# Kernel tuning notes

Hardware: AMD Instinct MI355X
Metric: run time of the kernel (lower is better)

## Reference

```python
import math
import jax, jax.numpy as jnp
import numpy as np

B, T, C, H, D = 2, 2048, 1024, 16, 64


def make_rope_cache(seq_len, head_dim, base=10000.0):
    half = head_dim // 2
    inv_freq = 1.0 / (base ** (np.arange(0, half, dtype=np.float32) / half))
    t = np.arange(seq_len, dtype=np.float32)
    freqs = np.outer(t, inv_freq)  # (T, D/2)
    cache = np.stack([np.cos(freqs), np.sin(freqs)], axis=1)  # (T, 2, D/2)
    return jnp.asarray(cache, dtype=jnp.float32)


def setup_inputs() -> dict:
    key = jax.random.key(0)
    ks = jax.random.split(key, 6)
    s = 1.0 / math.sqrt(C)
    return {
        "x": jax.random.normal(ks[0], (B, T, C), dtype=jnp.float32),
        "rope_cache": make_rope_cache(T, D),
        "Wq": jax.random.normal(ks[1], (C, C), dtype=jnp.float32) * s,
        "Wk": jax.random.normal(ks[2], (C, C), dtype=jnp.float32) * s,
        "Wv": jax.random.normal(ks[3], (C, C), dtype=jnp.float32) * s,
        "Wo": jax.random.normal(ks[4], (C, C), dtype=jnp.float32) * s,
        "mask": jnp.ones((B, T), dtype=jnp.bool_),
    }


def apply_rope(x, rope_cache):
    # x: (B, T, H, D); rope_cache: (T, 2, D//2)
    seq_len = x.shape[1]
    cos = rope_cache[:seq_len, 0, :][None, :, None, :]
    sin = rope_cache[:seq_len, 1, :][None, :, None, :]
    half = x.shape[-1] // 2
    x1, x2 = x[..., :half], x[..., half:]
    return jnp.concatenate([x1 * cos - x2 * sin, x1 * sin + x2 * cos], axis=-1)


def reference(x, rope_cache, Wq, Wk, Wv, Wo, mask):
    b, t, c = x.shape
    q = (x @ Wq).reshape(b, t, H, D)
    k = (x @ Wk).reshape(b, t, H, D)
    v = (x @ Wv).reshape(b, t, H, D)
    q = apply_rope(q, rope_cache).transpose(0, 2, 1, 3)  # (B,H,T,D)
    k = apply_rope(k, rope_cache).transpose(0, 2, 1, 3)
    v = v.transpose(0, 2, 1, 3)
    scale = 1.0 / math.sqrt(D)
    attn = jnp.einsum('bhid,bhjd->bhij', q, k) * scale  # (B,H,T,T)
    causal = jnp.tril(jnp.ones((t, t), dtype=jnp.bool_))
    attn = jnp.where(causal[None, None, :, :], attn, -1e9)
    attn = jnp.where(mask[:, None, None, :], attn, -1e9)
    attn = jax.nn.softmax(attn, axis=-1)
    out = jnp.einsum('bhij,bhjd->bhid', attn, v)
    out = out.transpose(0, 2, 1, 3).reshape(b, t, c)
    return out @ Wo
```

## Files before the change

kernel.cpp:

```cpp
#include <hip/hip_runtime.h>


typedef short s16x8 __attribute__((ext_vector_type(8)));
typedef __bf16 bf16x8 __attribute__((ext_vector_type(8)));
typedef float f32x4 __attribute__((ext_vector_type(4)));
typedef float f32x16 __attribute__((ext_vector_type(16)));
typedef unsigned u32x4 __attribute__((ext_vector_type(4)));
typedef unsigned u32x2 __attribute__((ext_vector_type(2)));

__device__ __forceinline__ short f2bf(float f) {
  unsigned u = __builtin_bit_cast(unsigned, f);
  u += 0x7fffu + ((u >> 16) & 1u);
  return (short)(u >> 16);
}

__device__ __forceinline__ unsigned cvtpk(float lo, float hi) {
  unsigned r;
  asm("v_cvt_pk_bf16_f32 %0, %1, %2" : "=v"(r) : "v"(lo), "v"(hi));
  return r;
}

__device__ __forceinline__ f32x4 mfma16(s16x8 a, s16x8 b, f32x4 c) {
  return __builtin_amdgcn_mfma_f32_16x16x32_bf16(
      __builtin_bit_cast(bf16x8, a), __builtin_bit_cast(bf16x8, b), c, 0, 0, 0);
}

__device__ __forceinline__ f32x16 mfma32(s16x8 a, s16x8 b, f32x16 c) {
  return __builtin_amdgcn_mfma_f32_32x32x16_bf16(
      __builtin_bit_cast(bf16x8, a), __builtin_bit_cast(bf16x8, b), c, 0, 0, 0);
}

__device__ __forceinline__ void gload16(const void* g, void* l) {
  __builtin_amdgcn_global_load_lds(
      (__attribute__((address_space(1))) void*)(void*)g,
      (__attribute__((address_space(3))) void*)l, 16, 0, 0);
}

__global__ void cvt_fused_kernel(const float* __restrict__ xin,
                                 const float* __restrict__ Wq, const float* __restrict__ Wk,
                                 const float* __restrict__ Wv, const float* __restrict__ Wo,
                                 short* __restrict__ xb, short* __restrict__ wt) {
  __shared__ float t32[32][33];
  int bid = blockIdx.x;
  int tid = threadIdx.x;
  if (bid < 2048) {
    int i = bid * 256 + tid;
    const float4* p = (const float4*)xin + (size_t)i * 2;
    float4 a = p[0], b = p[1];
    s16x8 o;
    o[0] = f2bf(a.x); o[1] = f2bf(a.y); o[2] = f2bf(a.z); o[3] = f2bf(a.w);
    o[4] = f2bf(b.x); o[5] = f2bf(b.y); o[6] = f2bf(b.z); o[7] = f2bf(b.w);
    ((s16x8*)xb)[i] = o;
  } else {
    int b = bid - 2048;
    int z = b >> 10;
    int rem = b & 1023;
    int n0 = (rem & 31) * 32, k0 = (rem >> 5) * 32;
    const float* W = (z == 0) ? Wq : (z == 1) ? Wk : (z == 2) ? Wv : Wo;
    short* o = wt + (size_t)z * 1024 * 1024;
    int tx = tid & 31, ty = tid >> 5;
#pragma unroll
    for (int i = 0; i < 4; ++i) t32[ty + 8 * i][tx] = W[(size_t)(k0 + ty + 8 * i) * 1024 + n0 + tx];
    __syncthreads();
#pragma unroll
    for (int i = 0; i < 4; ++i) o[(size_t)(n0 + ty + 8 * i) * 1024 + k0 + tx] = f2bf(t32[tx][ty + 8 * i]);
  }
}

__global__ __launch_bounds__(256) void qkv_gemm_kernel(
    const short* __restrict__ xb, const short* __restrict__ wt,
    const float* __restrict__ rope,
    short* __restrict__ Qo, short* __restrict__ Ko, short* __restrict__ Vt) {
  __shared__ short As[2][128 * 64];
  __shared__ short Bs[2][64 * 64];
  int bid = blockIdx.x;
  int wgid = (bid & 7) * 192 + (bid >> 3);
  int mt = wgid / 48;
  int ntile = wgid % 48;
  int mat = ntile >> 4;
  int h = ntile & 15;
  int tid = threadIdx.x, lane = tid & 63, w = tid >> 6;
  int rloc = lane & 15, lgrp = lane >> 4;
  int e3 = rloc & 7;

  const char* Agb0 = (const char*)(xb + (size_t)mt * 128 * 1024);
  const char* Bgb0 = (const char*)(wt + (size_t)mat * 1024 * 1024 + (size_t)h * 64 * 1024);

  f32x4 acc[2][4];
#pragma unroll
  for (int m = 0; m < 2; ++m)
#pragma unroll
    for (int n = 0; n < 4; ++n) acc[m][n] = (f32x4){0.f, 0.f, 0.f, 0.f};

  auto STAGE = [&](int buf, int kt) {
    const char* Ag = Agb0 + kt * 128;
    const char* Bg = Bgb0 + kt * 128;
    char* ad = (char*)&As[buf][0];
    char* bd = (char*)&Bs[buf][0];
#pragma unroll
    for (int rr = 0; rr < 4; ++rr) {
      int lin = rr * 4096 + tid * 16;
      int row = lin >> 7;
      int ch = (lin >> 4) & 7;
      int srcoff = (row << 11) + ((ch ^ (row & 7)) << 4);
      gload16(Ag + srcoff, ad + lin);
    }
#pragma unroll
    for (int rr = 0; rr < 2; ++rr) {
      int lin = rr * 4096 + tid * 16;
      int row = lin >> 7;
      int ch = (lin >> 4) & 7;
      int srcoff = (row << 11) + ((ch ^ (row & 7)) << 4);
      gload16(Bg + srcoff, bd + lin);
    }
  };

  STAGE(0, 0);
  for (int kt = 0; kt < 16; ++kt) {
    int cur = kt & 1;
    if (kt + 1 < 16) {
      STAGE(cur ^ 1, kt + 1);
      asm volatile("s_waitcnt vmcnt(6)" ::: "memory");
    } else {
      asm volatile("s_waitcnt vmcnt(0)" ::: "memory");
    }
    __builtin_amdgcn_s_barrier();
#pragma unroll
    for (int kk = 0; kk < 2; ++kk) {
      s16x8 a[2], b[4];
#pragma unroll
      for (int m = 0; m < 2; ++m)
        a[m] = *(const s16x8*)&As[cur][(w * 32 + m * 16 + rloc) * 64 + (((kk * 4 + lgrp) ^ e3) << 3)];
#pragma unroll
      for (int n = 0; n < 4; ++n)
        b[n] = *(const s16x8*)&Bs[cur][(n * 16 + rloc) * 64 + (((kk * 4 + lgrp) ^ e3) << 3)];
      __builtin_amdgcn_s_setprio(1);
#pragma unroll
      for (int m = 0; m < 2; ++m)
#pragma unroll
        for (int n = 0; n < 4; ++n) acc[m][n] = mfma16(a[m], b[n], acc[m][n]);
      __builtin_amdgcn_s_setprio(0);
    }
    __builtin_amdgcn_s_barrier();
  }

  if (mat < 2) {
    bool isK = (mat == 1);
    float csf = isK ? 1.0f : (0.125f * 1.44269504088896340736f);
    short* dst = (mat == 0) ? Qo : Ko;
#pragma unroll
    for (int m = 0; m < 2; ++m) {
#pragma unroll
      for (int j = 0; j < 4; ++j) {
        int rowg = mt * 128 + w * 32 + m * 16 + lgrp * 4 + j;
        int bI = rowg >> 11, t = rowg & 2047;
        short* hb = dst + (((size_t)(bI * 16 + h)) * 2048 + t) * 64;
#pragma unroll
        for (int n = 0; n < 2; ++n) {
          int d = n * 16 + rloc;
          float cs = rope[t * 64 + d] * csf;
          float sn = rope[t * 64 + 32 + d] * csf;
          float a0 = acc[m][n][j], b0 = acc[m][n + 2][j];
          int d2 = d + 32;
          int a1 = isK ? ((((d >> 3) ^ (t & 7)) << 3) | (d & 7)) : d;
          int a2 = isK ? ((((d2 >> 3) ^ (t & 7)) << 3) | (d & 7)) : d2;
          hb[a1] = f2bf(a0 * cs - b0 * sn);
          hb[a2] = f2bf(a0 * sn + b0 * cs);
        }
      }
    }
  } else {
    __syncthreads();
    short* T = &As[0][0];
#pragma unroll
    for (int m = 0; m < 2; ++m)
#pragma unroll
      for (int j = 0; j < 4; ++j) {
        int t_in = w * 32 + m * 16 + lgrp * 4 + j;
#pragma unroll
        for (int n = 0; n < 4; ++n) {
          int d = n * 16 + rloc;
          T[t_in * 66 + d] = f2bf(acc[m][n][j]);
        }
      }
    __syncthreads();
    int d = tid & 63;
    int th = tid >> 6;
    int t0g = mt * 128;
    int bI = t0g >> 11;
    short* vrow = Vt + (((size_t)(bI * 16 + h)) * 64 + d) * 2048 + (t0g & 2047);
#pragma unroll
    for (int c = 0; c < 4; ++c) {
      int tw0 = th * 32 + c * 8;
      s16x8 pk;
#pragma unroll
      for (int i = 0; i < 8; ++i) pk[i] = T[(tw0 + i) * 66 + d];
      int gr = (((tw0 >> 3) & 15) ^ (d & 15)) << 3;
      *(s16x8*)(vrow + gr) = pk;
    }
  }
}

__global__ __launch_bounds__(256, 2) void attn_kernel(
    const short* __restrict__ Q, const short* __restrict__ K,
    const short* __restrict__ Vt, short* __restrict__ O) {
  __shared__ short Ks[4][64 * 64];
  __shared__ short Vs[4][64 * 64];
  int tid = threadIdx.x;
  int lane = tid & 63;
  int w = tid >> 6;
  int bh = blockIdx.x;
  int qb = 15 - (int)blockIdx.y;
  int qv = lane & 31, h = lane >> 5;
  int q0 = qb * 128 + w * 32;
  int tq = q0 + qv;

  const short* Qg = Q + ((size_t)bh * 2048 + q0) * 64;
  s16x8 qf[4];
#pragma unroll
  for (int kq = 0; kq < 4; ++kq)
    qf[kq] = *(const s16x8*)(Qg + qv * 64 + kq * 16 + h * 8);

  const char* KgB = (const char*)(K + (size_t)bh * 2048 * 64);
  const char* VgB = (const char*)(Vt + (size_t)bh * 64 * 2048);

  f32x16 l_acc;
  f32x16 ot0, ot1;
#pragma unroll
  for (int r = 0; r < 16; ++r) { ot0[r] = 0.f; ot1[r] = 0.f; l_acc[r] = 0.f; }

  int nkv = 2 * qb + 2;

  auto STAGE = [&](int slot, int kt) {
    int k0 = kt << 6;
    const char* Kg = KgB + (size_t)k0 * 128;
    char* kd = (char*)&Ks[slot][0];
    char* vd = (char*)&Vs[slot][0];
    gload16(Kg + tid * 16, kd + tid * 16);
    gload16(Kg + 4096 + tid * 16, kd + 4096 + tid * 16);
    size_t vwin = (size_t)((k0 & ~127) * 2);
    int kpar = (k0 >> 6) & 1;
    {
      int lin = tid * 16;
      int d = lin >> 7, col = lin & 127;
      int ho = (((d >> 3) & 1) ^ kpar) << 7;
      gload16(VgB + (size_t)d * 4096 + vwin + ho + col, vd + lin);
    }
    {
      int lin = 4096 + tid * 16;
      int d = lin >> 7, col = lin & 127;
      int ho = (((d >> 3) & 1) ^ kpar) << 7;
      gload16(VgB + (size_t)d * 4096 + vwin + ho + col, vd + lin);
    }
  };

  STAGE(0, 0);
  STAGE(1, 1);

  for (int kt = 0; kt < nkv; ++kt) {
    int b = kt & 3;
    int k0 = kt << 6;
    if (kt + 2 < nkv) STAGE((kt + 2) & 3, kt + 2);
    if (kt + 2 < nkv)      asm volatile("s_waitcnt vmcnt(8)" ::: "memory");
    else if (kt + 1 < nkv) asm volatile("s_waitcnt vmcnt(4)" ::: "memory");
    else                   asm volatile("s_waitcnt vmcnt(0)" ::: "memory");
    __builtin_amdgcn_s_barrier();

    bool act = (k0 <= q0 + 31);
    if (act) {
      f32x16 s[2];
#pragma unroll
      for (int n = 0; n < 2; ++n)
#pragma unroll
        for (int r = 0; r < 16; ++r) s[n][r] = 0.f;
      __builtin_amdgcn_s_setprio(1);
#pragma unroll
      for (int n = 0; n < 2; ++n) {
        int r = n * 32 + qv;
#pragma unroll
        for (int kq = 0; kq < 4; ++kq) {
          s16x8 ka = *(const s16x8*)&Ks[b][r * 64 + (((2 * kq + h) ^ (r & 7)) << 3)];
          s[n] = mfma32(ka, qf[kq], s[n]);
        }
      }
      __builtin_amdgcn_s_setprio(0);
      if (k0 + 63 > q0) {
#pragma unroll
        for (int n = 0; n < 2; ++n)
#pragma unroll
          for (int r = 0; r < 16; ++r) {
            int tk = k0 + n * 32 + (r & 3) + ((r >> 2) << 3) + h * 4;
            if (tk > tq) s[n][r] = -3.0e38f;
          }
      }
#pragma unroll
      for (int n = 0; n < 2; ++n)
#pragma unroll
        for (int r = 0; r < 16; ++r)
          s[n][r] = exp2f(s[n][r]);
      l_acc += s[0] + s[1];

#pragma unroll
      for (int n = 0; n < 2; ++n) {
        unsigned dA[4], dB[4];
#pragma unroll
        for (int m = 0; m < 4; ++m) {
          dA[m] = cvtpk(s[n][4 * m], s[n][4 * m + 1]);
          dB[m] = cvtpk(s[n][4 * m + 2], s[n][4 * m + 3]);
        }
#pragma unroll
        for (int c = 0; c < 2; ++c) {
          u32x4 fv;
#if __has_builtin(__builtin_amdgcn_permlane32_swap)
          u32x2 pa = __builtin_amdgcn_permlane32_swap(dA[2 * c], dA[2 * c + 1], false, false);
          u32x2 pb = __builtin_amdgcn_permlane32_swap(dB[2 * c], dB[2 * c + 1], false, false);
          fv[0] = pa[0]; fv[1] = pb[0]; fv[2] = pa[1]; fv[3] = pb[1];
#else
          unsigned sendA = h ? dA[2 * c] : dA[2 * c + 1];
          unsigned sendB = h ? dB[2 * c] : dB[2 * c + 1];
          unsigned ownA  = h ? dA[2 * c + 1] : dA[2 * c];
          unsigned ownB  = h ? dB[2 * c + 1] : dB[2 * c];
          unsigned rA = (unsigned)__shfl_xor((int)sendA, 32);
          unsigned rB = (unsigned)__shfl_xor((int)sendB, 32);
          fv[0] = h ? rA : ownA;
          fv[1] = h ? rB : ownB;
          fv[2] = h ? ownA : rA;
          fv[3] = h ? ownB : rB;
#endif
          s16x8 pf = __builtin_bit_cast(s16x8, fv);
          int kk = 2 * n + c;
          int slot = ((2 * kk + h) ^ (qv & 7)) << 3;
          s16x8 va0 = *(const s16x8*)&Vs[b][qv * 64 + slot];
          s16x8 va1 = *(const s16x8*)&Vs[b][(32 + qv) * 64 + slot];
          __builtin_amdgcn_s_setprio(1);
          ot0 = mfma32(va0, pf, ot0);
          ot1 = mfma32(va1, pf, ot1);
          __builtin_amdgcn_s_setprio(0);
        }
      }
    }
  }

  float r8[8];
#pragma unroll
  for (int i = 0; i < 8; ++i) r8[i] = l_acc[i] + l_acc[i + 8];
#pragma unroll
  for (int off = 4; off > 0; off >>= 1)
#pragma unroll
    for (int i = 0; i < 4; ++i)
      if (i < off) r8[i] += r8[i + off];
  float l_run = r8[0];
  float l_tot = l_run + __shfl_xor(l_run, 32);
  float inv = 1.0f / l_tot;
  int bI = bh >> 4, h16 = bh & 15;
  short* Og = O + ((size_t)bI * 2048 + tq) * 1024 + h16 * 64;
#pragma unroll
  for (int r = 0; r < 16; r += 2) {
    int d = (r & 3) + ((r >> 2) << 3) + h * 4;
    *(unsigned*)(Og + d)      = cvtpk(ot0[r] * inv, ot0[r + 1] * inv);
    *(unsigned*)(Og + 32 + d) = cvtpk(ot1[r] * inv, ot1[r + 1] * inv);
  }
}

__global__ __launch_bounds__(256) void out_gemm_kernel(
    const short* __restrict__ Ob, const short* __restrict__ wto,
    float* __restrict__ out) {
  __shared__ short As[2][128 * 64];
  __shared__ short Bs[2][64 * 64];
  int bid = blockIdx.x;
  int wgid = (bid & 7) * 64 + (bid >> 3);
  int mt = wgid >> 4, nt = wgid & 15;
  int tid = threadIdx.x, lane = tid & 63, w = tid >> 6;
  int rloc = lane & 15, lgrp = lane >> 4;
  int e3 = rloc & 7;

  const char* Agb0 = (const char*)(Ob + (size_t)mt * 128 * 1024);
  const char* Bgb0 = (const char*)(wto + (size_t)nt * 64 * 1024);

  f32x4 acc[2][4];
#pragma unroll
  for (int m = 0; m < 2; ++m)
#pragma unroll
    for (int n = 0; n < 4; ++n) acc[m][n] = (f32x4){0.f, 0.f, 0.f, 0.f};

  auto STAGE = [&](int buf, int kt) {
    const char* Ag = Agb0 + kt * 128;
    const char* Bg = Bgb0 + kt * 128;
    char* ad = (char*)&As[buf][0];
    char* bd = (char*)&Bs[buf][0];
#pragma unroll
    for (int rr = 0; rr < 4; ++rr) {
      int lin = rr * 4096 + tid * 16;
      int row = lin >> 7;
      int ch = (lin >> 4) & 7;
      int srcoff = (row << 11) + ((ch ^ (row & 7)) << 4);
      gload16(Ag + srcoff, ad + lin);
    }
#pragma unroll
    for (int rr = 0; rr < 2; ++rr) {
      int lin = rr * 4096 + tid * 16;
      int row = lin >> 7;
      int ch = (lin >> 4) & 7;
      int srcoff = (row << 11) + ((ch ^ (row & 7)) << 4);
      gload16(Bg + srcoff, bd + lin);
    }
  };

  STAGE(0, 0);
  for (int kt = 0; kt < 16; ++kt) {
    int cur = kt & 1;
    if (kt + 1 < 16) {
      STAGE(cur ^ 1, kt + 1);
      asm volatile("s_waitcnt vmcnt(6)" ::: "memory");
    } else {
      asm volatile("s_waitcnt vmcnt(0)" ::: "memory");
    }
    __builtin_amdgcn_s_barrier();
#pragma unroll
    for (int kk = 0; kk < 2; ++kk) {
      s16x8 a[2], b[4];
#pragma unroll
      for (int m = 0; m < 2; ++m)
        a[m] = *(const s16x8*)&As[cur][(w * 32 + m * 16 + rloc) * 64 + (((kk * 4 + lgrp) ^ e3) << 3)];
#pragma unroll
      for (int n = 0; n < 4; ++n)
        b[n] = *(const s16x8*)&Bs[cur][(n * 16 + rloc) * 64 + (((kk * 4 + lgrp) ^ e3) << 3)];
      __builtin_amdgcn_s_setprio(1);
#pragma unroll
      for (int m = 0; m < 2; ++m)
#pragma unroll
        for (int n = 0; n < 4; ++n) acc[m][n] = mfma16(a[m], b[n], acc[m][n]);
      __builtin_amdgcn_s_setprio(0);
    }
    __builtin_amdgcn_s_barrier();
  }

#pragma unroll
  for (int m = 0; m < 2; ++m)
#pragma unroll
    for (int j = 0; j < 4; ++j) {
      int rowg = mt * 128 + w * 32 + m * 16 + lgrp * 4 + j;
#pragma unroll
      for (int n = 0; n < 4; ++n) {
        int colg = nt * 64 + n * 16 + rloc;
        out[(size_t)rowg * 1024 + colg] = acc[m][n][j];
      }
    }
}

extern "C" void kernel_launch(void* const* d_in, const int* in_sizes, int n_in,
                              void* d_out, int out_size, void* d_ws, size_t ws_size,
                              hipStream_t stream) {
  const float* x    = (const float*)d_in[0];
  const float* rope = (const float*)d_in[1];
  const float* Wq   = (const float*)d_in[2];
  const float* Wk   = (const float*)d_in[3];
  const float* Wv   = (const float*)d_in[4];
  const float* Wo   = (const float*)d_in[5];

  char* ws = (char*)d_ws;
  short* xb  = (short*)(ws);
  short* wt  = (short*)(ws + ((size_t)8  << 20));
  short* Qb  = (short*)(ws + ((size_t)16 << 20));
  short* Kb  = (short*)(ws + ((size_t)24 << 20));
  short* Vtb = (short*)(ws + ((size_t)32 << 20));
  short* Ob  = (short*)(ws + ((size_t)40 << 20));

  cvt_fused_kernel<<<6144, 256, 0, stream>>>(x, Wq, Wk, Wv, Wo, xb, wt);
  qkv_gemm_kernel<<<1536, 256, 0, stream>>>(xb, wt, rope, Qb, Kb, Vtb);
  attn_kernel<<<dim3(32, 16), 256, 0, stream>>>(Qb, Kb, Vtb, Ob);
  out_gemm_kernel<<<512, 256, 0, stream>>>(Ob, wt + (size_t)3 * 1024 * 1024, (float*)d_out);
}
```

Before: 107.0 us.

## Use 4-slot ring buffer with prefetch distance 2 and K-tile 32 in QKV GEMM

Restructures the QKV projection GEMM main loop from a double-buffered K=64 tile to a 4-slot ring of K=32 tiles with two stages in flight. The trailing barrier per iteration is removed, and the swizzle is changed to match the narrower 64-byte rows. The aim is to hide global load latency better and cut barriers per unit of work. In exchange there are twice as many iterations, each with fewer MFMAs between waits, and the LDS layout and bank pattern change. The extra slots are meant to make overwriting a slot safe without the second barrier.

```diff
diff --git a/kernel.cpp b/kernel.cpp
--- a/kernel.cpp
+++ b/kernel.cpp
@@ -71,8 +71,7 @@
     const short* __restrict__ xb, const short* __restrict__ wt,
     const float* __restrict__ rope,
     short* __restrict__ Qo, short* __restrict__ Ko, short* __restrict__ Vt) {
-  __shared__ short As[2][128 * 64];
-  __shared__ short Bs[2][64 * 64];
+  __shared__ short S[4 * 4096 + 4 * 2048];
   int bid = blockIdx.x;
   int wgid = (bid & 7) * 192 + (bid >> 3);
   int mt = wgid / 48;
@@ -81,7 +80,6 @@
   int h = ntile & 15;
   int tid = threadIdx.x, lane = tid & 63, w = tid >> 6;
   int rloc = lane & 15, lgrp = lane >> 4;
-  int e3 = rloc & 7;
 
   const char* Agb0 = (const char*)(xb + (size_t)mt * 128 * 1024);
   const char* Bgb0 = (const char*)(wt + (size_t)mat * 1024 * 1024 + (size_t)h * 64 * 1024);
@@ -92,56 +90,55 @@
 #pragma unroll
     for (int n = 0; n < 4; ++n) acc[m][n] = (f32x4){0.f, 0.f, 0.f, 0.f};
 
-  auto STAGE = [&](int buf, int kt) {
-    const char* Ag = Agb0 + kt * 128;
-    const char* Bg = Bgb0 + kt * 128;
-    char* ad = (char*)&As[buf][0];
-    char* bd = (char*)&Bs[buf][0];
-#pragma unroll
-    for (int rr = 0; rr < 4; ++rr) {
-      int lin = rr * 4096 + tid * 16;
-      int row = lin >> 7;
-      int ch = (lin >> 4) & 7;
-      int srcoff = (row << 11) + ((ch ^ (row & 7)) << 4);
-      gload16(Ag + srcoff, ad + lin);
-    }
+  auto STAGE = [&](int slot, int kt) {
+    const char* Ag = Agb0 + kt * 64;
+    const char* Bg = Bgb0 + kt * 64;
+    char* ad = (char*)(S + slot * 4096);
+    char* bd = (char*)(S + 16384 + slot * 2048);
 #pragma unroll
     for (int rr = 0; rr < 2; ++rr) {
       int lin = rr * 4096 + tid * 16;
-      int row = lin >> 7;
-      int ch = (lin >> 4) & 7;
-      int srcoff = (row << 11) + ((ch ^ (row & 7)) << 4);
+      int row = lin >> 6;
+      int ch = (lin >> 4) & 3;
+      int srcoff = (row << 11) + ((ch ^ ((row >> 1) & 3)) << 4);
+      gload16(Ag + srcoff, ad + lin);
+    }
+    {
+      int lin = tid * 16;
+      int row = lin >> 6;
+      int ch = (lin >> 4) & 3;
+      int srcoff = (row << 11) + ((ch ^ ((row >> 1) & 3)) << 4);
       gload16(Bg + srcoff, bd + lin);
     }
   };
 
   STAGE(0, 0);
-  for (int kt = 0; kt < 16; ++kt) {
-    int cur = kt & 1;
-    if (kt + 1 < 16) {
-      STAGE(cur ^ 1, kt + 1);
-      asm volatile("s_waitcnt vmcnt(6)" ::: "memory");
-    } else {
-      asm volatile("s_waitcnt vmcnt(0)" ::: "memory");
-    }
+  STAGE(1, 1);
+  for (int kt = 0; kt < 32; ++kt) {
+    int sl = kt & 3;
+    if (kt + 2 < 32) STAGE((kt + 2) & 3, kt + 2);
+    if (kt + 2 < 32)      asm volatile("s_waitcnt vmcnt(6)" ::: "memory");
+    else if (kt + 1 < 32) asm volatile("s_waitcnt vmcnt(3)" ::: "memory");
+    else                  asm volatile("s_waitcnt vmcnt(0)" ::: "memory");
     __builtin_amdgcn_s_barrier();
-#pragma unroll
-    for (int kk = 0; kk < 2; ++kk) {
-      s16x8 a[2], b[4];
-#pragma unroll
-      for (int m = 0; m < 2; ++m)
-        a[m] = *(const s16x8*)&As[cur][(w * 32 + m * 16 + rloc) * 64 + (((kk * 4 + lgrp) ^ e3) << 3)];
-#pragma unroll
-      for (int n = 0; n < 4; ++n)
-        b[n] = *(const s16x8*)&Bs[cur][(n * 16 + rloc) * 64 + (((kk * 4 + lgrp) ^ e3) << 3)];
-      __builtin_amdgcn_s_setprio(1);
-#pragma unroll
-      for (int m = 0; m < 2; ++m)
-#pragma unroll
-        for (int n = 0; n < 4; ++n) acc[m][n] = mfma16(a[m], b[n], acc[m][n]);
-      __builtin_amdgcn_s_setprio(0);
-    }
-    __builtin_amdgcn_s_barrier();
+
+    s16x8 a[2], b[4];
+#pragma unroll
+    for (int m = 0; m < 2; ++m) {
+      int row = w * 32 + m * 16 + rloc;
+      a[m] = *(const s16x8*)&S[sl * 4096 + row * 32 + ((lgrp ^ ((row >> 1) & 3)) << 3)];
+    }
+#pragma unroll
+    for (int n = 0; n < 4; ++n) {
+      int row = n * 16 + rloc;
+      b[n] = *(const s16x8*)&S[16384 + sl * 2048 + row * 32 + ((lgrp ^ ((row >> 1) & 3)) << 3)];
+    }
+    __builtin_amdgcn_s_setprio(1);
+#pragma unroll
+    for (int m = 0; m < 2; ++m)
+#pragma unroll
+      for (int n = 0; n < 4; ++n) acc[m][n] = mfma16(a[m], b[n], acc[m][n]);
+    __builtin_amdgcn_s_setprio(0);
   }
 
   if (mat < 2) {
@@ -171,7 +168,7 @@
     }
   } else {
     __syncthreads();
-    short* T = &As[0][0];
+    short* T = S;
 #pragma unroll
     for (int m = 0; m < 2; ++m)
 #pragma unroll
```

After: 119.7 us. 11.9% more time.
